# Optimization experiments

Hardware: AMD Instinct MI355X
Metric: run time of the kernel (lower is better)

Reference implementation:

```python
import jax, jax.numpy as jnp
import numpy as np

B, CIN, H, W = 1, 128, 448, 512
CLASSES = 128
CR0, CR1 = 128, 4


def setup_inputs() -> dict:
    key = jax.random.key(0)
    ks = jax.random.split(key, 13)
    s = 0.05  # small init scale to keep leaky_relu chain numerically tame
    def rn(k, shape):
        return jax.random.normal(k, shape, dtype=jnp.float32) * s
    return {
        "x_in": jax.random.normal(ks[0], (B, CIN, H, W), dtype=jnp.float32),
        # grouped 1x1 convs, groups=height -> per-height (out, in) matrices
        "w_cl1": rn(ks[1], (H, 128, CIN)), "b_cl1": rn(ks[2], (H, 128)),
        "w_cl2": rn(ks[3], (H, 128, 128)), "b_cl2": rn(ks[4], (H, 128)),
        "w_cl3": rn(ks[5], (H, CLASSES + 1, 128)), "b_cl3": rn(ks[6], (H, CLASSES + 1)),
        "w_reg1": rn(ks[7], (H, CR0, CIN)), "b_reg1": rn(ks[8], (H, CR0)),
        # CondMul expert tables: one small matmul per (height, class) index
        "w2": rn(ks[9], (H * CLASSES, CR0, CR1)), "b2": rn(ks[10], (H * CLASSES, CR1)),
        "w3": rn(ks[11], (H * CLASSES, CR1, 1)), "b3": rn(ks[12], (H * CLASSES, 1)),
    }


def _lrelu(v):
    return jnp.where(v >= 0, v, 0.01 * v)


def _gconv(t, wt, bt):
    # grouped 1x1 conv with groups=height: per-height matmul over channels
    # t: (B,H,Cin,W), wt: (H,Cout,Cin), bt: (H,Cout) -> (B,H,Cout,W)
    return jnp.einsum('bhcw,hoc->bhow', t, wt) + bt[None, :, :, None]


def reference(x_in, w_cl1, b_cl1, w_cl2, b_cl2, w_cl3, b_cl3,
              w_reg1, b_reg1, w2, b2, w3, b3):
    b, _, h, w = x_in.shape
    n_cls = w_cl3.shape[1] - 1
    x = jnp.transpose(x_in, (0, 2, 1, 3))  # (B,H,Cin,W)

    x_r = _lrelu(_gconv(x, w_reg1, b_reg1))  # (B,H,CR0,W)
    t = _lrelu(_gconv(x, w_cl1, b_cl1))
    t = _lrelu(_gconv(t, w_cl2, b_cl2))
    cl = jnp.transpose(_gconv(t, w_cl3, b_cl3), (0, 2, 1, 3))  # (B,classes+1,H,W)

    logits = cl[:, :n_cls]          # (B,classes,H,W)
    mask = _lrelu(cl[:, -1:])       # (B,1,H,W)
    inds = jnp.argmax(logits, axis=1)  # (B,H,W) hard routing

    # indices flattened in (b,h,w) order (as in the original)
    inds_r = (inds + jnp.arange(h)[None, :, None] * n_cls).reshape(-1).astype(jnp.int32)
    rows = jnp.transpose(x_r, (0, 3, 1, 2)).reshape(-1, x_r.shape[2])  # (N,CR0)

    # CondMul: per-row expert gather + tiny matmul + bias
    hdn = _lrelu(jnp.einsum('nc,nco->no', rows, w2[inds_r]) + b2[inds_r])  # (N,CR1)
    r = jnp.einsum('nc,nco->no', hdn, w3[inds_r]) + b3[inds_r]             # (N,1)
    r = jnp.transpose(r.reshape(b, w, h, 1), (0, 3, 2, 1))  # (B,1,H,W)

    x_real = (inds[:, None].astype(jnp.float32) + r) * (1.0 / float(n_cls))
    return (x_real, mask)
```

## Files before the change

kernel.cpp:

```cpp
#include <hip/hip_runtime.h>
#include <hip/hip_bf16.h>

#define HH 448
#define WW 512
#define CHW (HH*WW)
#define NPIX (HH*WW)
#define WCH 128
#define LDW 140

typedef unsigned short u16;
typedef __attribute__((ext_vector_type(8))) u16 ushort8v;

__device__ __forceinline__ float lrelu(float v) { return v >= 0.f ? v : 0.01f * v; }

__device__ __forceinline__ u16 f2bf(float v) {
    __hip_bfloat16 b = __float2bfloat16(v);
    union { __hip_bfloat16 h; u16 u; } cv; cv.h = b;
    return cv.u;
}

__device__ __forceinline__ float bf2f(u16 u) {
    union { unsigned int i; float f; } cv; cv.i = ((unsigned int)u) << 16;
    return cv.f;
}

__device__ __forceinline__ int swz8(int g) { return g * 8 + ((g >> 2) << 2); }

template<bool EXTRA>
__device__ __forceinline__ void gemm_phase(
    const float* __restrict__ wsrc, const float* __restrict__ bsrc, int O,
    const float* __restrict__ xs, float* __restrict__ biasb,
    float (&acc)[8][8], float& a128, int tid, int o0, int xoff, int swtid)
{
#pragma unroll
    for (int i = 0; i < 8; ++i)
#pragma unroll
        for (int j = 0; j < 8; ++j) acc[i][j] = 0.f;
    a128 = 0.f;

    __syncthreads();
    if (tid < O) biasb[tid] = bsrc[tid];

    const float* wb   = wsrc + o0 * 128;
    const float* w128 = wsrc + 128 * 128;

#pragma unroll 2
    for (int k4 = 0; k4 < 32; ++k4) {
        float4 wv[8];
#pragma unroll
        for (int i = 0; i < 8; ++i)
            wv[i] = *(const float4*)(wb + i * 128 + k4 * 4);
        float4 xva[4], xvb[4];
#pragma unroll
        for (int r = 0; r < 4; ++r) {
            xva[r] = *(const float4*)(xs + (k4 * 4 + r) * LDW + xoff);
            xvb[r] = *(const float4*)(xs + (k4 * 4 + r) * LDW + xoff + 4);
        }
#pragma unroll
        for (int r = 0; r < 4; ++r) {
            const float xr8[8] = {xva[r].x, xva[r].y, xva[r].z, xva[r].w,
                                  xvb[r].x, xvb[r].y, xvb[r].z, xvb[r].w};
#pragma unroll
            for (int i = 0; i < 8; ++i) {
                const float ws4[4] = {wv[i].x, wv[i].y, wv[i].z, wv[i].w};
                const float wi = ws4[r];
#pragma unroll
                for (int j = 0; j < 8; ++j)
                    acc[i][j] = fmaf(wi, xr8[j], acc[i][j]);
            }
        }
        if (EXTRA && tid < 128) {
            const float4 w4 = *(const float4*)(w128 + k4 * 4);
            a128 = fmaf(w4.x, xs[(k4 * 4 + 0) * LDW + swtid], a128);
            a128 = fmaf(w4.y, xs[(k4 * 4 + 1) * LDW + swtid], a128);
            a128 = fmaf(w4.z, xs[(k4 * 4 + 2) * LDW + swtid], a128);
            a128 = fmaf(w4.w, xs[(k4 * 4 + 3) * LDW + swtid], a128);
        }
    }

    __syncthreads();
}

__global__ __launch_bounds__(256, 2) void stage1_kernel(
    const float* __restrict__ x_in,
    const float* __restrict__ w_cl1, const float* __restrict__ b_cl1,
    const float* __restrict__ w_cl2, const float* __restrict__ b_cl2,
    const float* __restrict__ w_cl3, const float* __restrict__ b_cl3,
    const float* __restrict__ w_reg1, const float* __restrict__ b_reg1,
    u16* __restrict__ xr_ws, int* __restrict__ inds_ws, float* __restrict__ out)
{
    __shared__ float xs[128 * LDW];
    __shared__ float biasb[132];

    const int tid = threadIdx.x;
    const int b = blockIdx.x;
    const int h     = (b >> 5) * 8 + (b & 7);
    const int chunk = (b >> 3) & 3;
    const int wbase = chunk * WCH;

    const int og = tid >> 4, wg = tid & 15;
    const int o0 = og * 8,  w0 = wg * 8;
    const int xoff  = swz8(wg);
    const int swtid = swz8(tid >> 3) + (tid & 7);

    {
        const float* xg = x_in + h * WW + wbase;
#pragma unroll
        for (int it = 0; it < 16; ++it) {
            int slot = it * 256 + tid;
            int c = slot >> 5, w4 = slot & 31;
            float4 v = *(const float4*)(xg + (size_t)c * CHW + w4 * 4);
            *(float4*)(xs + c * LDW + swz8(w4 >> 1) + (w4 & 1) * 4) = v;
        }
    }

    float acc[8][8]; float a128;

    gemm_phase<false>(w_reg1 + (size_t)h * 16384, b_reg1 + h * 128, 128, xs, biasb, acc, a128, tid, o0, xoff, swtid);
    {
#pragma unroll
        for (int j = 0; j < 8; ++j) {
            const int n = (wbase + w0 + j) * HH + h;
            ushort8v pk;
#pragma unroll
            for (int i = 0; i < 8; ++i)
                pk[i] = f2bf(lrelu(acc[i][j] + biasb[o0 + i]));
            *(ushort8v*)(xr_ws + (size_t)n * 128 + o0) = pk;
        }
    }

    gemm_phase<false>(w_cl1 + (size_t)h * 16384, b_cl1 + h * 128, 128, xs, biasb, acc, a128, tid, o0, xoff, swtid);
#pragma unroll
    for (int i = 0; i < 8; ++i) {
        float bo = biasb[o0 + i];
        *(float4*)(xs + (o0 + i) * LDW + xoff) =
            make_float4(lrelu(acc[i][0] + bo), lrelu(acc[i][1] + bo), lrelu(acc[i][2] + bo), lrelu(acc[i][3] + bo));
        *(float4*)(xs + (o0 + i) * LDW + xoff + 4) =
            make_float4(lrelu(acc[i][4] + bo), lrelu(acc[i][5] + bo), lrelu(acc[i][6] + bo), lrelu(acc[i][7] + bo));
    }

    gemm_phase<false>(w_cl2 + (size_t)h * 16384, b_cl2 + h * 128, 128, xs, biasb, acc, a128, tid, o0, xoff, swtid);
#pragma unroll
    for (int i = 0; i < 8; ++i) {
        float bo = biasb[o0 + i];
        *(float4*)(xs + (o0 + i) * LDW + xoff) =
            make_float4(lrelu(acc[i][0] + bo), lrelu(acc[i][1] + bo), lrelu(acc[i][2] + bo), lrelu(acc[i][3] + bo));
        *(float4*)(xs + (o0 + i) * LDW + xoff + 4) =
            make_float4(lrelu(acc[i][4] + bo), lrelu(acc[i][5] + bo), lrelu(acc[i][6] + bo), lrelu(acc[i][7] + bo));
    }

    gemm_phase<true>(w_cl3 + (size_t)h * 16512, b_cl3 + h * 129, 129, xs, biasb, acc, a128, tid, o0, xoff, swtid);

    float* sval = xs;
    int*   sidx = (int*)(xs + 2048);
#pragma unroll
    for (int j = 0; j < 8; ++j) {
        float bv = -3.4e38f; int bi = 0;
#pragma unroll
        for (int i = 0; i < 8; ++i) {
            float v = acc[i][j] + biasb[o0 + i];
            if (v > bv) { bv = v; bi = o0 + i; }
        }
        sval[og * 128 + (w0 + j)] = bv;
        sidx[og * 128 + (w0 + j)] = bi;
    }
    __syncthreads();
    if (tid < 128) {
        const int w = tid;
        float bv = sval[w]; int bi = sidx[w];
#pragma unroll
        for (int g = 1; g < 16; ++g) {
            float v = sval[g * 128 + w];
            if (v > bv) { bv = v; bi = sidx[g * 128 + w]; }
        }
        inds_ws[h * WW + wbase + w] = bi;
        out[NPIX + h * WW + wbase + w] = lrelu(a128 + biasb[128]);
    }
}

__global__ __launch_bounds__(256, 4) void stage2_kernel(
    const u16* __restrict__ xr_ws, const int* __restrict__ inds_ws,
    const float* __restrict__ w2g, const float* __restrict__ b2g,
    const float* __restrict__ w3g, const float* __restrict__ b3g,
    float* __restrict__ out)
{
    const int lane = threadIdx.x & 63;
    const int n = blockIdx.x * 4 + (threadIdx.x >> 6);
    const unsigned un = (unsigned)n;
    const int h = un % 448u, w = un / 448u;
    const int idx = inds_ws[n] + ((n >> 9) << 7);

    const int c0 = lane << 1;
    const u16* rp = xr_ws + (size_t)n * 128 + c0;
    const float r0 = bf2f(rp[0]), r1 = bf2f(rp[1]);

    const float* wrow = w2g + (size_t)idx * 512;
    const float4 wa = *(const float4*)(wrow + (c0 << 2));
    const float4 wb = *(const float4*)(wrow + (c0 << 2) + 4);

    float s0 = r0 * wa.x + r1 * wb.x;
    float s1 = r0 * wa.y + r1 * wb.y;
    float s2 = r0 * wa.z + r1 * wb.z;
    float s3 = r0 * wa.w + r1 * wb.w;
#pragma unroll
    for (int m = 1; m < 64; m <<= 1) {
        s0 += __shfl_xor(s0, m, 64);
        s1 += __shfl_xor(s1, m, 64);
        s2 += __shfl_xor(s2, m, 64);
        s3 += __shfl_xor(s3, m, 64);
    }
    if (lane == 0) {
        const float4 b2v = *(const float4*)(b2g + (idx << 2));
        const float4 w3v = *(const float4*)(w3g + (idx << 2));
        float rr = b3g[idx];
        rr += lrelu(s0 + b2v.x) * w3v.x;
        rr += lrelu(s1 + b2v.y) * w3v.y;
        rr += lrelu(s2 + b2v.z) * w3v.z;
        rr += lrelu(s3 + b2v.w) * w3v.w;
        const int p = h * WW + w;
        const float ind_local = (float)inds_ws[p];
        out[p] = (ind_local + rr) * 0.0078125f;
    }
}

extern "C" void kernel_launch(void* const* d_in, const int* in_sizes, int n_in,
                              void* d_out, int out_size, void* d_ws, size_t ws_size,
                              hipStream_t stream)
{
    const float* x_in   = (const float*)d_in[0];
    const float* w_cl1  = (const float*)d_in[1];
    const float* b_cl1  = (const float*)d_in[2];
    const float* w_cl2  = (const float*)d_in[3];
    const float* b_cl2  = (const float*)d_in[4];
    const float* w_cl3  = (const float*)d_in[5];
    const float* b_cl3  = (const float*)d_in[6];
    const float* w_reg1 = (const float*)d_in[7];
    const float* b_reg1 = (const float*)d_in[8];
    const float* w2     = (const float*)d_in[9];
    const float* b2     = (const float*)d_in[10];
    const float* w3     = (const float*)d_in[11];
    const float* b3     = (const float*)d_in[12];

    float* out = (float*)d_out;
    u16* xr_ws = (u16*)d_ws;
    int* inds  = (int*)((char*)d_ws + (size_t)NPIX * 128 * 2);

    stage1_kernel<<<dim3(448 * 4), dim3(256), 0, stream>>>(
        x_in, w_cl1, b_cl1, w_cl2, b_cl2, w_cl3, b_cl3, w_reg1, b_reg1,
        xr_ws, inds, out);

    stage2_kernel<<<dim3(NPIX / 4), dim3(256), 0, stream>>>(
        xr_ws, inds, w2, b2, w3, b3, out);
}
```

Baseline: 671.5 us.

## Process eight rows per wavefront in stage2 and add LDS barriers in stage1

Stage2 now gives each pixel row to eight lanes instead of a full 64-lane wavefront. Each lane loads 16 bf16 activations as vectors and runs a serial FMA loop over its chunk, then a three-step shuffle reduction replaces the six-step one. The per-row bias and weight loads are issued early, and the grid shrinks eightfold. Stage1 gains __syncthreads barriers before the shared tile is overwritten after each GEMM phase, which fixes a possible read/write race but adds synchronisation cost.

```diff
diff --git a/kernel.cpp b/kernel.cpp
--- a/kernel.cpp
+++ b/kernel.cpp
@@ -130,6 +130,7 @@
     }
 
     gemm_phase<false>(w_cl1 + (size_t)h * 16384, b_cl1 + h * 128, 128, xs, biasb, acc, a128, tid, o0, xoff, swtid);
+    __syncthreads();
 #pragma unroll
     for (int i = 0; i < 8; ++i) {
         float bo = biasb[o0 + i];
@@ -140,6 +141,7 @@
     }
 
     gemm_phase<false>(w_cl2 + (size_t)h * 16384, b_cl2 + h * 128, 128, xs, biasb, acc, a128, tid, o0, xoff, swtid);
+    __syncthreads();
 #pragma unroll
     for (int i = 0; i < 8; ++i) {
         float bo = biasb[o0 + i];
@@ -151,6 +153,7 @@
 
     gemm_phase<true>(w_cl3 + (size_t)h * 16512, b_cl3 + h * 129, 129, xs, biasb, acc, a128, tid, o0, xoff, swtid);
 
+    __syncthreads();
     float* sval = xs;
     int*   sidx = (int*)(xs + 2048);
 #pragma unroll
@@ -184,42 +187,56 @@
     const float* __restrict__ w3g, const float* __restrict__ b3g,
     float* __restrict__ out)
 {
-    const int lane = threadIdx.x & 63;
-    const int n = blockIdx.x * 4 + (threadIdx.x >> 6);
+    const int l  = threadIdx.x & 63;
+    const int wv = threadIdx.x >> 6;
+    const int nl = l >> 3, cg = l & 7;
+    const int n  = blockIdx.x * 32 + wv * 8 + nl;
     const unsigned un = (unsigned)n;
     const int h = un % 448u, w = un / 448u;
     const int idx = inds_ws[n] + ((n >> 9) << 7);
 
-    const int c0 = lane << 1;
+    float4 b2v = make_float4(0.f, 0.f, 0.f, 0.f);
+    float4 w3v = make_float4(0.f, 0.f, 0.f, 0.f);
+    float  b3s = 0.f;
+    int    indp = 0;
+    const int p = h * WW + w;
+    if (cg == 0) {
+        b2v  = *(const float4*)(b2g + (idx << 2));
+        w3v  = *(const float4*)(w3g + (idx << 2));
+        b3s  = b3g[idx];
+        indp = inds_ws[p];
+    }
+
+    const int c0 = cg << 4;
     const u16* rp = xr_ws + (size_t)n * 128 + c0;
-    const float r0 = bf2f(rp[0]), r1 = bf2f(rp[1]);
-
-    const float* wrow = w2g + (size_t)idx * 512;
-    const float4 wa = *(const float4*)(wrow + (c0 << 2));
-    const float4 wb = *(const float4*)(wrow + (c0 << 2) + 4);
-
-    float s0 = r0 * wa.x + r1 * wb.x;
-    float s1 = r0 * wa.y + r1 * wb.y;
-    float s2 = r0 * wa.z + r1 * wb.z;
-    float s3 = r0 * wa.w + r1 * wb.w;
-#pragma unroll
-    for (int m = 1; m < 64; m <<= 1) {
+    const ushort8v x0 = *(const ushort8v*)(rp);
+    const ushort8v x1 = *(const ushort8v*)(rp + 8);
+
+    const float* wrow = w2g + (size_t)idx * 512 + (c0 << 2);
+    float s0 = 0.f, s1 = 0.f, s2 = 0.f, s3 = 0.f;
+#pragma unroll
+    for (int t = 0; t < 16; ++t) {
+        const float4 w4 = *(const float4*)(wrow + t * 4);
+        const float xc = bf2f(t < 8 ? x0[t] : x1[t - 8]);
+        s0 = fmaf(xc, w4.x, s0);
+        s1 = fmaf(xc, w4.y, s1);
+        s2 = fmaf(xc, w4.z, s2);
+        s3 = fmaf(xc, w4.w, s3);
+    }
+#pragma unroll
+    for (int m = 1; m < 8; m <<= 1) {
         s0 += __shfl_xor(s0, m, 64);
         s1 += __shfl_xor(s1, m, 64);
         s2 += __shfl_xor(s2, m, 64);
         s3 += __shfl_xor(s3, m, 64);
     }
-    if (lane == 0) {
-        const float4 b2v = *(const float4*)(b2g + (idx << 2));
-        const float4 w3v = *(const float4*)(w3g + (idx << 2));
-        float rr = b3g[idx];
+    if (cg == 0) {
+        float rr = b3s;
         rr += lrelu(s0 + b2v.x) * w3v.x;
         rr += lrelu(s1 + b2v.y) * w3v.y;
         rr += lrelu(s2 + b2v.z) * w3v.z;
         rr += lrelu(s3 + b2v.w) * w3v.w;
-        const int p = h * WW + w;
-        const float ind_local = (float)inds_ws[p];
-        out[p] = (ind_local + rr) * 0.0078125f;
+        out[p] = ((float)indp + rr) * 0.0078125f;
     }
 }
 
@@ -249,6 +266,6 @@
         x_in, w_cl1, b_cl1, w_cl2, b_cl2, w_cl3, b_cl3, w_reg1, b_reg1,
         xr_ws, inds, out);
 
-    stage2_kernel<<<dim3(NPIX / 4), dim3(256), 0, stream>>>(
+    stage2_kernel<<<dim3(NPIX / 32), dim3(256), 0, stream>>>(
         xr_ws, inds, w2, b2, w3, b3, out);
 }
```

Result: slower. 689.0 us (+2.6%).
